# Kernel tuning notes

Measured on AMD Instinct MI355X. Metric: run time of the kernel, lower is better.

## Reference

```python
import jax, jax.numpy as jnp
import numpy as np

N_HEAD_HALF = 8          # config.n_head // 2
LAMBDA_INIT = 0.2        # diff_lambda_init
RMS_EPS = 1.1920929e-07  # torch.finfo(float32).eps (F.rms_norm default)
ROPE_BASE = 10000.0


def setup_inputs() -> dict:
    key = jax.random.key(0)
    ks = jax.random.split(key, 9)
    B, T, C = 2, 2048, 2048
    HD = C // N_HEAD_HALF  # 256
    s = 0.02
    return {
        "x": jax.random.normal(ks[0], (B, T, C), jnp.float32),
        "wq": jax.random.normal(ks[1], (C, C), jnp.float32) * s,
        "wk": jax.random.normal(ks[2], (C, C), jnp.float32) * s,
        "wv": jax.random.normal(ks[3], (C, C), jnp.float32) * s,
        "wo": jax.random.normal(ks[4], (C, C), jnp.float32) * s,
        "lq1": jax.random.normal(ks[5], (HD,), jnp.float32) * 0.1,
        "lk1": jax.random.normal(ks[6], (HD,), jnp.float32) * 0.1,
        "lq2": jax.random.normal(ks[7], (HD,), jnp.float32) * 0.1,
        "lk2": jax.random.normal(ks[8], (HD,), jnp.float32) * 0.1,
    }


def _rms_norm(x):
    var = jnp.mean(x * x, axis=-1, keepdims=True)
    return x * jax.lax.rsqrt(var + RMS_EPS)


def _rotary(x):
    # Faithful to original bug: positions run along axis 1 (the HEAD axis),
    # since Rotary is applied after transpose(1,2). x: (B, NH, T, D)
    d = x.shape[-1]
    inv_freq = (1.0 / ROPE_BASE) ** (jnp.arange(0, d, 2, dtype=jnp.float32) / d)
    t = jnp.arange(x.shape[1], dtype=jnp.float32)
    freqs = jnp.outer(t, inv_freq)                      # (NH, d/2)
    cos = jnp.cos(freqs)[None, :, None, :]
    sin = jnp.sin(freqs)[None, :, None, :]
    x1, x2 = jnp.split(x, 2, axis=-1)
    return jnp.concatenate((x1 * cos + x2 * sin, -x1 * sin + x2 * cos), axis=-1)


def _causal_attn(q, k, v, scale):
    # q,k: (B,NH,T,Dh)  v: (B,NH,T,HD)
    T = q.shape[2]
    s = jnp.einsum("bhqd,bhkd->bhqk", q, k) * scale
    mask = jnp.tril(jnp.ones((T, T), dtype=bool))
    s = jnp.where(mask, s, jnp.float32(-jnp.inf))
    p = jax.nn.softmax(s, axis=-1)
    return jnp.einsum("bhqk,bhkd->bhqd", p, v)


def reference(x, wq, wk, wv, wo, lq1, lk1, lq2, lk2):
    B, T, C = x.shape
    NH = N_HEAD_HALF
    HD = C // NH
    HH = HD // 2

    lam1 = jnp.exp(jnp.sum(lq1 * lk1))
    lam2 = jnp.exp(jnp.sum(lq2 * lk2))
    lam = lam1 - lam2 + LAMBDA_INIT

    q = (x @ wq.T).reshape(B, T, NH, 2, HH).transpose(0, 2, 1, 3, 4)
    k = (x @ wk.T).reshape(B, T, NH, 2, HH).transpose(0, 2, 1, 3, 4)
    v = (x @ wv.T).reshape(B, T, NH, HD).transpose(0, 2, 1, 3)

    q1 = _rotary(_rms_norm(q[..., 0, :]))
    q2 = _rotary(_rms_norm(q[..., 1, :]))
    k1 = _rotary(_rms_norm(k[..., 0, :]))
    k2 = _rotary(_rms_norm(k[..., 1, :]))

    scale = 1.0 / jnp.sqrt(jnp.float32(HH))
    y = _causal_attn(q1, k1, v, scale) - lam * _causal_attn(q2, k2, v, scale)

    y = y.transpose(0, 2, 1, 3).reshape(B, T, C)
    y = (y @ wo.T) * (1.0 - LAMBDA_INIT)
    return y
```

## Files before the change

kernel.cpp:

```cpp
#include <hip/hip_runtime.h>
#include <hip/hip_bf16.h>

using bf16 = __hip_bfloat16;
typedef __bf16 bf16x8_t __attribute__((ext_vector_type(8)));
typedef __bf16 bf16x4_t __attribute__((ext_vector_type(4)));
typedef float f32x4  __attribute__((ext_vector_type(4)));
typedef float f32x16 __attribute__((ext_vector_type(16)));

#define AS1 __attribute__((address_space(1)))
#define AS3 __attribute__((address_space(3)))

__device__ __forceinline__ void gll16(const void* g, void* l) {
  __builtin_amdgcn_global_load_lds((const AS1 void*)g, (AS3 void*)l, 16u, 0, 0u);
}

__device__ __forceinline__ __bf16 tobf(float f) {
  bf16 h = __float2bfloat16(f);
  return __builtin_bit_cast(__bf16, h);
}

__global__ __launch_bounds__(256) void k_cvt(
    const float* __restrict__ x,  const float* __restrict__ wq,
    const float* __restrict__ wk, const float* __restrict__ wv,
    const float* __restrict__ wo,
    bf16* __restrict__ xb,  bf16* __restrict__ wqb, bf16* __restrict__ wkb,
    bf16* __restrict__ wvb, bf16* __restrict__ wob) {
  size_t id = (size_t)blockIdx.x * 256 + threadIdx.x;
  const float* s; bf16* d; size_t off;
  if (id < 2097152) { s = x; d = xb; off = id; }
  else {
    size_t r = id - 2097152;
    unsigned w = (unsigned)(r >> 20);
    off = r & 1048575u;
    s = (w == 0) ? wq : (w == 1) ? wk : (w == 2) ? wv : wo;
    d = (w == 0) ? wqb : (w == 1) ? wkb : (w == 2) ? wvb : wob;
  }
  const float4 v = ((const float4*)s)[off];
  bf16x4_t o = { tobf(v.x), tobf(v.y), tobf(v.z), tobf(v.w) };
  *(bf16x4_t*)(d + off * 4) = o;
}

__global__ __launch_bounds__(256) void k_lam(
    const float* __restrict__ lq1, const float* __restrict__ lk1,
    const float* __restrict__ lq2, const float* __restrict__ lk2,
    float* __restrict__ lam) {
  __shared__ float r1[4], r2[4];
  int t = threadIdx.x;
  float a = lq1[t] * lk1[t];
  float b = lq2[t] * lk2[t];
#pragma unroll
  for (int s = 1; s < 64; s <<= 1) { a += __shfl_xor(a, s); b += __shfl_xor(b, s); }
  if ((t & 63) == 0) { r1[t >> 6] = a; r2[t >> 6] = b; }
  __syncthreads();
  if (t == 0) {
    float s1 = r1[0] + r1[1] + r1[2] + r1[3];
    float s2 = r2[0] + r2[1] + r2[2] + r2[3];
    *lam = expf(s1) - expf(s2) + 0.2f;
  }
}

#define MFMA16(a, b, c) __builtin_amdgcn_mfma_f32_16x16x32_bf16(a, b, c, 0, 0, 0)

template<bool SWAP>
__device__ __forceinline__ void gemm256(
    const bf16* __restrict__ A, const bf16* __restrict__ B,
    int m0, int n0, bf16* lds, f32x4 (&acc)[8][4]) {
  const int tid = threadIdx.x, lane = tid & 63;
  const int wave = tid >> 6, m = wave >> 2, n = wave & 3;
  const int g = lane >> 4, l15 = lane & 15, l7 = lane & 7;

  const int sid0 = tid, sid1 = tid + 512;
  const int sr0 = sid0 >> 3, sc0 = (sid0 & 7) ^ (sr0 & 7);
  const int sr1 = sid1 >> 3, sc1 = (sid1 & 7) ^ (sr1 & 7);

  auto stageA = [&](int t, int h) {
    bf16* d = lds + ((size_t)((t & 1) * 2 + h)) * 8192;
    gll16(A + (size_t)(m0 + h * 128 + sr0) * 2048 + t * 64 + sc0 * 8, d + sid0 * 8);
    gll16(A + (size_t)(m0 + h * 128 + sr1) * 2048 + t * 64 + sc1 * 8, d + sid1 * 8);
  };
  auto stageB = [&](int t, int h) {
    bf16* d = lds + 32768 + ((size_t)((t & 1) * 2 + h)) * 8192;
    gll16(B + (size_t)(n0 + h * 128 + sr0) * 2048 + t * 64 + sc0 * 8, d + sid0 * 8);
    gll16(B + (size_t)(n0 + h * 128 + sr1) * 2048 + t * 64 + sc1 * 8, d + sid1 * 8);
  };

  stageA(0, 0); stageB(0, 0); stageB(0, 1); stageA(0, 1);
  stageA(1, 0); stageB(1, 0); stageB(1, 1);
  asm volatile("s_waitcnt vmcnt(6)\n\ts_barrier" ::: "memory");

  for (int t = 0; t < 32; ++t) {
    const bf16* lA0 = lds + ((size_t)((t & 1) * 2 + 0)) * 8192;
    const bf16* lA1 = lds + ((size_t)((t & 1) * 2 + 1)) * 8192;
    const bf16* lB0 = lds + 32768 + ((size_t)((t & 1) * 2 + 0)) * 8192;
    const bf16* lB1 = lds + 32768 + ((size_t)((t & 1) * 2 + 1)) * 8192;
    bf16x8_t afl[4][2], afh[4][2], bvl[2][2], bvh[2][2];

#pragma unroll
    for (int ks = 0; ks < 2; ++ks) {
      const int pc = ((ks * 4 + g) ^ l7) * 8;
#pragma unroll
      for (int rf = 0; rf < 4; ++rf)
        afl[rf][ks] = *(const bf16x8_t*)(lA0 + (m * 64 + rf * 16 + l15) * 64 + pc);
#pragma unroll
      for (int cf = 0; cf < 2; ++cf)
        bvl[cf][ks] = *(const bf16x8_t*)(lB0 + (cf * 64 + n * 16 + l15) * 64 + pc);
    }
    if (t + 1 < 32) stageA(t + 1, 1);
    asm volatile("s_barrier" ::: "memory");
    __builtin_amdgcn_s_setprio(1);
#pragma unroll
    for (int ks = 0; ks < 2; ++ks)
#pragma unroll
      for (int rf = 0; rf < 4; ++rf)
#pragma unroll
        for (int cf = 0; cf < 2; ++cf)
          acc[rf][cf] = SWAP ? MFMA16(bvl[cf][ks], afl[rf][ks], acc[rf][cf])
                             : MFMA16(afl[rf][ks], bvl[cf][ks], acc[rf][cf]);
    __builtin_amdgcn_s_setprio(0);
    asm volatile("s_barrier" ::: "memory");

#pragma unroll
    for (int ks = 0; ks < 2; ++ks) {
      const int pc = ((ks * 4 + g) ^ l7) * 8;
#pragma unroll
      for (int cf = 0; cf < 2; ++cf)
        bvh[cf][ks] = *(const bf16x8_t*)(lB1 + (cf * 64 + n * 16 + l15) * 64 + pc);
    }
    if (t + 2 < 32) stageA(t + 2, 0);
    asm volatile("s_barrier" ::: "memory");
    __builtin_amdgcn_s_setprio(1);
#pragma unroll
    for (int ks = 0; ks < 2; ++ks)
#pragma unroll
      for (int rf = 0; rf < 4; ++rf)
#pragma unroll
        for (int cf = 0; cf < 2; ++cf)
          acc[rf][cf + 2] = SWAP ? MFMA16(bvh[cf][ks], afl[rf][ks], acc[rf][cf + 2])
                                 : MFMA16(afl[rf][ks], bvh[cf][ks], acc[rf][cf + 2]);
    __builtin_amdgcn_s_setprio(0);
    asm volatile("s_barrier" ::: "memory");

#pragma unroll
    for (int ks = 0; ks < 2; ++ks) {
      const int pc = ((ks * 4 + g) ^ l7) * 8;
#pragma unroll
      for (int rf = 0; rf < 4; ++rf)
        afh[rf][ks] = *(const bf16x8_t*)(lA1 + (m * 64 + rf * 16 + l15) * 64 + pc);
    }
    if (t + 2 < 32) stageB(t + 2, 0);
    asm volatile("s_barrier" ::: "memory");
    __builtin_amdgcn_s_setprio(1);
#pragma unroll
    for (int ks = 0; ks < 2; ++ks)
#pragma unroll
      for (int rf = 0; rf < 4; ++rf)
#pragma unroll
        for (int cf = 0; cf < 2; ++cf)
          acc[rf + 4][cf + 2] = SWAP ? MFMA16(bvh[cf][ks], afh[rf][ks], acc[rf + 4][cf + 2])
                                     : MFMA16(afh[rf][ks], bvh[cf][ks], acc[rf + 4][cf + 2]);
    __builtin_amdgcn_s_setprio(0);
    asm volatile("s_barrier" ::: "memory");

    if (t + 2 < 32) stageB(t + 2, 1);
    asm volatile("s_barrier" ::: "memory");
    __builtin_amdgcn_s_setprio(1);
#pragma unroll
    for (int ks = 0; ks < 2; ++ks)
#pragma unroll
      for (int rf = 0; rf < 4; ++rf)
#pragma unroll
        for (int cf = 0; cf < 2; ++cf)
          acc[rf + 4][cf] = SWAP ? MFMA16(bvl[cf][ks], afh[rf][ks], acc[rf + 4][cf])
                                 : MFMA16(afh[rf][ks], bvl[cf][ks], acc[rf + 4][cf]);
    __builtin_amdgcn_s_setprio(0);
    if (t < 30)      asm volatile("s_waitcnt vmcnt(6)\n\ts_barrier" ::: "memory");
    else             asm volatile("s_waitcnt vmcnt(0)\n\ts_barrier" ::: "memory");
  }
}

__global__ __launch_bounds__(512, 2) void k_gemm_qkv(
    const bf16* __restrict__ xb,
    const bf16* __restrict__ wqb, const bf16* __restrict__ wkb,
    const bf16* __restrict__ wvb,
    bf16* __restrict__ q1, bf16* __restrict__ q2,
    bf16* __restrict__ k1, bf16* __restrict__ k2,
    bf16* __restrict__ vt) {
  __shared__ __align__(16) bf16 lds[65536];
  __shared__ float exs[2][4][256];
  __shared__ float lCs[64], lSn[64];
  const int z  = blockIdx.z;
  const int m0 = blockIdx.y * 256, n0 = blockIdx.x * 256;
  const int nh = blockIdx.x;
  const int tid = threadIdx.x, lane = tid & 63, wave = tid >> 6;
  const int m = wave >> 2, n = wave & 3;
  const int g = lane >> 4, l15 = lane & 15;
  f32x4 acc[8][4] = {};

  if (z < 2) {
    if (tid < 64) {
      float fr = exp2f(-(float)tid * 0.20762050593045951f);
      float sn, cs;
      sincosf((float)nh * fr, &sn, &cs);
      lCs[tid] = cs; lSn[tid] = sn;
    }
    const bf16* Bm = z ? wkb : wqb;
    gemm256<true>(xb, Bm, m0, n0, lds, acc);

#pragma unroll
    for (int rf = 0; rf < 8; ++rf) {
      float s0 = 0.f, s1 = 0.f;
#pragma unroll
      for (int r = 0; r < 4; ++r) {
        s0 += acc[rf][0][r] * acc[rf][0][r] + acc[rf][1][r] * acc[rf][1][r];
        s1 += acc[rf][2][r] * acc[rf][2][r] + acc[rf][3][r] * acc[rf][3][r];
      }
      s0 += __shfl_xor(s0, 16); s0 += __shfl_xor(s0, 32);
      s1 += __shfl_xor(s1, 16); s1 += __shfl_xor(s1, 32);
      const int rrow = (rf >> 2) * 128 + m * 64 + (rf & 3) * 16 + l15;
      if (g == 0) { exs[0][n][rrow] = s0; exs[1][n][rrow] = s1; }
    }
    __syncthreads();
    bf16* dst1 = z ? k1 : q1;
    bf16* dst2 = z ? k2 : q2;
    const int j = n * 16 + 4 * g;
#pragma unroll
    for (int rf = 0; rf < 8; ++rf) {
      const int rrow = (rf >> 2) * 128 + m * 64 + (rf & 3) * 16 + l15;
      const float t0 = exs[0][0][rrow] + exs[0][1][rrow] + exs[0][2][rrow] + exs[0][3][rrow];
      const float t1 = exs[1][0][rrow] + exs[1][1][rrow] + exs[1][2][rrow] + exs[1][3][rrow];
      const float inv0 = rsqrtf(t0 * (1.0f / 128.0f) + 1.1920929e-07f);
      const float inv1 = rsqrtf(t1 * (1.0f / 128.0f) + 1.1920929e-07f);
      const size_t base = ((size_t)(m0 + rrow) * 8 + nh) * 128;
      bf16x4_t o1a, o2a, o1b, o2b;
#pragma unroll
      for (int r = 0; r < 4; ++r) {
        const float cs = lCs[j + r], sn = lSn[j + r];
        float x1 = acc[rf][0][r] * inv0, x2 = acc[rf][1][r] * inv0;
        o1a[r] = tobf(x1 * cs + x2 * sn);
        o2a[r] = tobf(x2 * cs - x1 * sn);
        x1 = acc[rf][2][r] * inv1; x2 = acc[rf][3][r] * inv1;
        o1b[r] = tobf(x1 * cs + x2 * sn);
        o2b[r] = tobf(x2 * cs - x1 * sn);
      }
      *(bf16x4_t*)(dst1 + base + j)      = o1a;
      *(bf16x4_t*)(dst1 + base + j + 64) = o2a;
      *(bf16x4_t*)(dst2 + base + j)      = o1b;
      *(bf16x4_t*)(dst2 + base + j + 64) = o2b;
    }
  } else {
    gemm256<false>(xb, wvb, m0, n0, lds, acc);
#pragma unroll
    for (int rf = 0; rf < 8; ++rf)
#pragma unroll
      for (int cf = 0; cf < 4; ++cf) {
        const int rb = m0 + (rf >> 2) * 128 + m * 64 + (rf & 3) * 16 + 4 * g;
        const int hd = (cf & 1) * 64 + (cf >> 1) * 128 + n * 16 + l15;
        const int b = rb >> 11, t = rb & 2047;
        bf16x4_t pv;
#pragma unroll
        for (int r = 0; r < 4; ++r) pv[r] = tobf(acc[rf][cf][r]);
        *(bf16x4_t*)(vt + ((size_t)((b * 8 + nh) * 256 + hd)) * 2048 + t) = pv;
      }
  }
}

template<bool SWAP>
__device__ __forceinline__ void gemm_core(
    const bf16* __restrict__ A, const bf16* __restrict__ Bm,
    int m0, int n0, bf16* lA, bf16* lB, f32x4 (&acc)[4][4]) {
  const int tid  = threadIdx.x;
  const int lane = tid & 63;
  const int g    = lane >> 4;
  const int l15  = lane & 15;
  const int l7   = lane & 7;
  const int wave = tid >> 6;
  const int wm   = (wave >> 1) * 64;
  const int wn   = (wave & 1) * 64;

  int srow[4], ssc[4];
#pragma unroll
  for (int j = 0; j < 4; ++j) {
    int id = tid + j * 256;
    srow[j] = id >> 3;
    ssc[j]  = (id & 7) ^ (srow[j] & 7);
  }

  for (int k0 = 0; k0 < 2048; k0 += 64) {
    __syncthreads();
#pragma unroll
    for (int j = 0; j < 4; ++j) {
      int id = tid + j * 256;
      gll16(A  + (size_t)(m0 + srow[j]) * 2048 + k0 + ssc[j] * 8, lA + id * 8);
      gll16(Bm + (size_t)(n0 + srow[j]) * 2048 + k0 + ssc[j] * 8, lB + id * 8);
    }
    __syncthreads();
#pragma unroll
    for (int ks = 0; ks < 2; ++ks) {
      const int pc = (ks * 4 + g) ^ l7;
      bf16x8_t af[4], bfr[4];
#pragma unroll
      for (int mt = 0; mt < 4; ++mt)
        af[mt] = *(const bf16x8_t*)(lA + (wm + mt * 16 + l15) * 64 + pc * 8);
#pragma unroll
      for (int nt = 0; nt < 4; ++nt)
        bfr[nt] = *(const bf16x8_t*)(lB + (wn + nt * 16 + l15) * 64 + pc * 8);
#pragma unroll
      for (int mt = 0; mt < 4; ++mt)
#pragma unroll
        for (int nt = 0; nt < 4; ++nt) {
          if (SWAP)
            acc[mt][nt] = MFMA16(bfr[nt], af[mt], acc[mt][nt]);
          else
            acc[mt][nt] = MFMA16(af[mt], bfr[nt], acc[mt][nt]);
        }
    }
  }
}

__global__ __launch_bounds__(256) void k_gemm_out(
    const bf16* __restrict__ yb, const bf16* __restrict__ wob,
    float* __restrict__ outp) {
  __shared__ __align__(16) bf16 lA[128 * 64];
  __shared__ __align__(16) bf16 lB[128 * 64];
  const int m0 = blockIdx.y * 128, n0 = blockIdx.x * 128;
  f32x4 acc[4][4] = {};
  gemm_core<true>(yb, wob, m0, n0, lA, lB, acc);
  const int lane = threadIdx.x & 63, wave = threadIdx.x >> 6;
  const int g = lane >> 4, l15 = lane & 15;
  const int wm = (wave >> 1) * 64, wn = (wave & 1) * 64;
#pragma unroll
  for (int mt = 0; mt < 4; ++mt)
#pragma unroll
    for (int nt = 0; nt < 4; ++nt) {
      int row = m0 + wm + mt * 16 + l15;
      int col = n0 + wn + nt * 16 + 4 * g;
      f32x4 v;
#pragma unroll
      for (int r = 0; r < 4; ++r) v[r] = acc[mt][nt][r] * 0.8f;
      *(f32x4*)(outp + (size_t)row * 2048 + col) = v;
    }
}

__global__ __launch_bounds__(256, 1) void k_flash(
    const bf16* __restrict__ q1b, const bf16* __restrict__ q2b,
    const bf16* __restrict__ k1b, const bf16* __restrict__ k2b,
    const bf16* __restrict__ vtb, const float* __restrict__ lamp,
    bf16* __restrict__ yb) {
  __shared__ __align__(16) bf16 smem[65536];
  const int tid  = threadIdx.x;
  const int lane = tid & 63, wave = tid >> 6;
  const int pair = blockIdx.x;
  const int bh = blockIdx.y;
  const int b = bh >> 3, nh = bh & 7;
  const int at = wave & 1, qg = wave >> 1;
  const int l31 = lane & 31, g5 = lane >> 5, l7 = lane & 7;
  const float scale = 0.08838834764831845f;
  const float lam = *lamp;

  auto stage = [&](int kt, int buf) {
    bf16* dst = smem + buf * 32768;
    const int k0 = kt * 64;
#pragma unroll
    for (int it = 0; it < 4; ++it) {
      int id = tid + it * 256;
      int row = id >> 4, c = id & 15;
      int sc = (c & 8) | ((c & 7) ^ (row & 7));
      size_t goff = ((size_t)(b * 2048 + k0 + row) * 8 + nh) * 128 + sc * 8;
      gll16(k1b + goff, dst + id * 8);
      gll16(k2b + goff, dst + 8192 + id * 8);
    }
#pragma unroll
    for (int it = 0; it < 8; ++it) {
      int id = tid + it * 256;
      int row = id >> 3, c = id & 7;
      int sc = c ^ (row & 7);
      gll16(vtb + ((size_t)(bh * 256 + row)) * 2048 + k0 + sc * 8,
            dst + 16384 + id * 8);
    }
  };

  bf16x8_t qf[8];
  auto loadQ = [&](int qt) {
    int qglob = qt * 64 + qg * 32 + l31;
    const bf16* qp = (at ? q2b : q1b) +
                     ((size_t)(b * 2048 + qglob) * 8 + nh) * 128 + g5 * 8;
#pragma unroll
    for (int ks = 0; ks < 8; ++ks) qf[ks] = *(const bf16x8_t*)(qp + ks * 16);
  };

  f32x16 O[8];
  float mrun, lrun;
  auto resetO = [&]() {
#pragma unroll
    for (int i = 0; i < 8; ++i)
#pragma unroll
      for (int j = 0; j < 16; ++j) O[i][j] = 0.f;
    mrun = -1e30f; lrun = 0.f;
  };

  auto step = [&](int kt, int buf, int qt) {
    const bf16* lk = smem + buf * 32768 + (at ? 8192 : 0);
    const bf16* lv = smem + buf * 32768 + 16384;
    const int k0 = kt * 64;
    const int qglob = qt * 64 + qg * 32 + l31;

    f32x16 s0, s1;
#pragma unroll
    for (int j = 0; j < 16; ++j) { s0[j] = 0.f; s1[j] = 0.f; }
#pragma unroll
    for (int ks = 0; ks < 8; ++ks) {
      int cl = ks * 2 + g5;
      int pc = (cl & 8) | ((cl & 7) ^ l7);
      bf16x8_t a0 = *(const bf16x8_t*)(lk + l31 * 128 + pc * 8);
      bf16x8_t a1 = *(const bf16x8_t*)(lk + (32 + l31) * 128 + pc * 8);
      s0 = __builtin_amdgcn_mfma_f32_32x32x16_bf16(a0, qf[ks], s0, 0, 0, 0);
      s1 = __builtin_amdgcn_mfma_f32_32x32x16_bf16(a1, qf[ks], s1, 0, 0, 0);
    }

    const bool diag = (kt == qt);
    float rmax = -3.0e38f;
#pragma unroll
    for (int r = 0; r < 16; ++r) {
      int key0 = k0 + (r & 3) + 8 * (r >> 2) + 4 * g5;
      float v0 = s0[r] * scale;
      float v1 = s1[r] * scale;
      if (diag) {
        if (key0 > qglob)      v0 = -1e30f;
        if (key0 + 32 > qglob) v1 = -1e30f;
      }
      s0[r] = v0; s1[r] = v1;
      rmax = fmaxf(rmax, fmaxf(v0, v1));
    }
    rmax = fmaxf(rmax, __shfl_xor(rmax, 32));
    float mnew = fmaxf(mrun, rmax);
    float alpha = __expf(mrun - mnew);
    float psum = 0.f;
#pragma unroll
    for (int r = 0; r < 16; ++r) {
      float p0 = __expf(s0[r] - mnew);
      float p1 = __expf(s1[r] - mnew);
      s0[r] = p0; s1[r] = p1;
      psum += p0 + p1;
    }
    psum += __shfl_xor(psum, 32);
    lrun = lrun * alpha + psum;
    mrun = mnew;
#pragma unroll
    for (int i = 0; i < 8; ++i) O[i] *= alpha;

#pragma unroll
    for (int sl = 0; sl < 4; ++sl) {
      const int h = sl & 1;
      bf16x4_t lo, hi;
#pragma unroll
      for (int j = 0; j < 4; ++j) {
        float vl = (sl < 2) ? s0[h * 8 + j]     : s1[h * 8 + j];
        float vh = (sl < 2) ? s0[h * 8 + 4 + j] : s1[h * 8 + 4 + j];
        lo[j] = tobf(vl); hi[j] = tobf(vh);
      }
      bf16x4_t send = g5 ? lo : hi;
      int2 si = __builtin_bit_cast(int2, send);
      int2 ri;
      ri.x = __shfl_xor(si.x, 32);
      ri.y = __shfl_xor(si.y, 32);
      bf16x4_t recv = __builtin_bit_cast(bf16x4_t, ri);
      bf16x4_t f0 = g5 ? recv : lo;
      bf16x4_t f1 = g5 ? hi : recv;
      bf16x8_t pf = { f0[0], f0[1], f0[2], f0[3], f1[0], f1[1], f1[2], f1[3] };

      const int cl = sl * 2 + g5;
#pragma unroll
      for (int mt = 0; mt < 8; ++mt) {
        bf16x8_t vf = *(const bf16x8_t*)(lv + (mt * 32 + l31) * 64 + (cl ^ l7) * 8);
        O[mt] = __builtin_amdgcn_mfma_f32_32x32x16_bf16(vf, pf, O[mt], 0, 0, 0);
      }
    }
  };

  auto finish = [&](int qt, bf16* cb) {
    const int qglob = qt * 64 + qg * 32 + l31;
    const float invl = 1.f / lrun;
    __syncthreads();
    if (at) {
      const float f = lam * invl;
#pragma unroll
      for (int mt = 0; mt < 8; ++mt)
#pragma unroll
        for (int rq = 0; rq < 4; ++rq) {
          int hd = mt * 32 + 8 * rq + 4 * g5;
          bf16x4_t pv;
#pragma unroll
          for (int i = 0; i < 4; ++i) pv[i] = tobf(O[mt][rq * 4 + i] * f);
          *(bf16x4_t*)(cb + (size_t)(qg * 32 + l31) * 264 + hd) = pv;
        }
    }
    __syncthreads();
    if (!at) {
#pragma unroll
      for (int mt = 0; mt < 8; ++mt)
#pragma unroll
        for (int rq = 0; rq < 4; ++rq) {
          int hd = mt * 32 + 8 * rq + 4 * g5;
          bf16x4_t o2 = *(const bf16x4_t*)(cb + (size_t)(qg * 32 + l31) * 264 + hd);
          bf16x4_t pv;
#pragma unroll
          for (int i = 0; i < 4; ++i)
            pv[i] = tobf(O[mt][rq * 4 + i] * invl - (float)o2[i]);
          *(bf16x4_t*)(yb + (size_t)(b * 2048 + qglob) * 2048 + nh * 256 + hd) = pv;
        }
    }
  };

  const int qtB = 31 - pair, qtA = pair;

  loadQ(qtB);
  resetO();
  stage(0, 0);
  for (int kt = 0; kt <= qtB; ++kt) {
    __syncthreads();
    if (kt < qtB) stage(kt + 1, (kt + 1) & 1);
    else          stage(0, (kt + 1) & 1);
    step(kt, kt & 1, qtB);
  }
  finish(qtB, smem + (qtB & 1) * 32768);

  loadQ(qtA);
  resetO();
  for (int kt = 0; kt <= qtA; ++kt) {
    __syncthreads();
    if (kt < qtA) stage(kt + 1, (qtB + kt + 2) & 1);
    step(kt, (qtB + 1 + kt) & 1, qtA);
  }
  finish(qtA, smem + 32768);
}

extern "C" void kernel_launch(void* const* d_in, const int* in_sizes, int n_in,
                              void* d_out, int out_size, void* d_ws, size_t ws_size,
                              hipStream_t stream) {
  (void)in_sizes; (void)n_in; (void)out_size; (void)ws_size;
  const float* x   = (const float*)d_in[0];
  const float* wq  = (const float*)d_in[1];
  const float* wk  = (const float*)d_in[2];
  const float* wv  = (const float*)d_in[3];
  const float* wo  = (const float*)d_in[4];
  const float* lq1 = (const float*)d_in[5];
  const float* lk1 = (const float*)d_in[6];
  const float* lq2 = (const float*)d_in[7];
  const float* lk2 = (const float*)d_in[8];
  float* out = (float*)d_out;

  char* p = (char*)d_ws;
  float* lam = (float*)p;            p += 256;
  bf16* xb  = (bf16*)p;              p += (size_t)4096 * 2048 * 2;
  bf16* wqb = (bf16*)p;              p += (size_t)2048 * 2048 * 2;
  bf16* wkb = (bf16*)p;              p += (size_t)2048 * 2048 * 2;
  bf16* wvb = (bf16*)p;              p += (size_t)2048 * 2048 * 2;
  bf16* wob = (bf16*)p;              p += (size_t)2048 * 2048 * 2;
  bf16* vt  = (bf16*)p;              p += (size_t)4096 * 2048 * 2;
  bf16* q1b = (bf16*)p;              p += (size_t)4096 * 1024 * 2;
  bf16* q2b = (bf16*)p;              p += (size_t)4096 * 1024 * 2;
  bf16* k1b = (bf16*)p;              p += (size_t)4096 * 1024 * 2;
  bf16* k2b = (bf16*)p;              p += (size_t)4096 * 1024 * 2;
  bf16* yb  = (bf16*)p;              p += (size_t)4096 * 2048 * 2;

  k_cvt<<<24576, 256, 0, stream>>>(x, wq, wk, wv, wo, xb, wqb, wkb, wvb, wob);
  k_lam<<<1, 256, 0, stream>>>(lq1, lk1, lq2, lk2, lam);
  k_gemm_qkv<<<dim3(8, 16, 3), 512, 0, stream>>>(xb, wqb, wkb, wvb,
                                                 q1b, q2b, k1b, k2b, vt);
  k_flash<<<dim3(16, 16), 256, 0, stream>>>(q1b, q2b, k1b, k2b, vt, lam, yb);
  k_gemm_out<<<dim3(16, 32), 256, 0, stream>>>(yb, wob, out);
}
```

Baseline: 434.0 us.

## Split flash attention KV tile across two wave groups with lazy rescaling

Doubles the flash-attention block to 512 threads. Each 64-key tile is split into two 32-key halves handled by separate wave groups, and the two partial softmax states are merged through shared memory at the end. Adds an exp2 with the scale folded into log2e, skips fully masked half-tiles, and only rescales the running max when it grows by more than a threshold. This raises the number of waves per CU and cuts per-wave register pressure, at the cost of an extra merge with more barriers and shared-memory traffic.

```diff
diff --git a/kernel.cpp b/kernel.cpp
--- a/kernel.cpp
+++ b/kernel.cpp
@@ -341,28 +341,29 @@
     }
 }
 
-__global__ __launch_bounds__(256, 1) void k_flash(
+__global__ __launch_bounds__(512, 2) void k_flash(
     const bf16* __restrict__ q1b, const bf16* __restrict__ q2b,
     const bf16* __restrict__ k1b, const bf16* __restrict__ k2b,
     const bf16* __restrict__ vtb, const float* __restrict__ lamp,
     bf16* __restrict__ yb) {
   __shared__ __align__(16) bf16 smem[65536];
+  __shared__ float mx[8][32], lx[8][32];
   const int tid  = threadIdx.x;
   const int lane = tid & 63, wave = tid >> 6;
   const int pair = blockIdx.x;
   const int bh = blockIdx.y;
   const int b = bh >> 3, nh = bh & 7;
-  const int at = wave & 1, qg = wave >> 1;
+  const int at = wave & 1, qg = (wave >> 1) & 1, kvh = wave >> 2;
   const int l31 = lane & 31, g5 = lane >> 5, l7 = lane & 7;
-  const float scale = 0.08838834764831845f;
+  const float sl2e = 0.12751743f;
   const float lam = *lamp;
 
   auto stage = [&](int kt, int buf) {
     bf16* dst = smem + buf * 32768;
     const int k0 = kt * 64;
 #pragma unroll
-    for (int it = 0; it < 4; ++it) {
-      int id = tid + it * 256;
+    for (int it = 0; it < 2; ++it) {
+      int id = tid + it * 512;
       int row = id >> 4, c = id & 15;
       int sc = (c & 8) | ((c & 7) ^ (row & 7));
       size_t goff = ((size_t)(b * 2048 + k0 + row) * 8 + nh) * 128 + sc * 8;
@@ -370,8 +371,8 @@
       gll16(k2b + goff, dst + 8192 + id * 8);
     }
 #pragma unroll
-    for (int it = 0; it < 8; ++it) {
-      int id = tid + it * 256;
+    for (int it = 0; it < 4; ++it) {
+      int id = tid + it * 512;
       int row = id >> 3, c = id & 7;
       int sc = c ^ (row & 7);
       gll16(vtb + ((size_t)(bh * 256 + row)) * 2048 + k0 + sc * 8,
@@ -399,64 +400,61 @@
   };
 
   auto step = [&](int kt, int buf, int qt) {
+    const int k0 = kt * 64 + kvh * 32;
+    if (k0 > qt * 64 + qg * 32 + 31) return;
     const bf16* lk = smem + buf * 32768 + (at ? 8192 : 0);
     const bf16* lv = smem + buf * 32768 + 16384;
-    const int k0 = kt * 64;
     const int qglob = qt * 64 + qg * 32 + l31;
 
-    f32x16 s0, s1;
-#pragma unroll
-    for (int j = 0; j < 16; ++j) { s0[j] = 0.f; s1[j] = 0.f; }
+    f32x16 s0;
+#pragma unroll
+    for (int j = 0; j < 16; ++j) s0[j] = 0.f;
 #pragma unroll
     for (int ks = 0; ks < 8; ++ks) {
       int cl = ks * 2 + g5;
       int pc = (cl & 8) | ((cl & 7) ^ l7);
-      bf16x8_t a0 = *(const bf16x8_t*)(lk + l31 * 128 + pc * 8);
-      bf16x8_t a1 = *(const bf16x8_t*)(lk + (32 + l31) * 128 + pc * 8);
+      bf16x8_t a0 = *(const bf16x8_t*)(lk + (kvh * 32 + l31) * 128 + pc * 8);
       s0 = __builtin_amdgcn_mfma_f32_32x32x16_bf16(a0, qf[ks], s0, 0, 0, 0);
-      s1 = __builtin_amdgcn_mfma_f32_32x32x16_bf16(a1, qf[ks], s1, 0, 0, 0);
-    }
-
-    const bool diag = (kt == qt);
+    }
+
+    const bool needmask = (k0 + 31 > qt * 64 + qg * 32);
     float rmax = -3.0e38f;
 #pragma unroll
     for (int r = 0; r < 16; ++r) {
-      int key0 = k0 + (r & 3) + 8 * (r >> 2) + 4 * g5;
-      float v0 = s0[r] * scale;
-      float v1 = s1[r] * scale;
-      if (diag) {
-        if (key0 > qglob)      v0 = -1e30f;
-        if (key0 + 32 > qglob) v1 = -1e30f;
-      }
-      s0[r] = v0; s1[r] = v1;
-      rmax = fmaxf(rmax, fmaxf(v0, v1));
+      float v0 = s0[r] * sl2e;
+      if (needmask) {
+        int key0 = k0 + (r & 3) + 8 * (r >> 2) + 4 * g5;
+        if (key0 > qglob) v0 = -1e30f;
+      }
+      s0[r] = v0;
+      rmax = fmaxf(rmax, v0);
     }
     rmax = fmaxf(rmax, __shfl_xor(rmax, 32));
-    float mnew = fmaxf(mrun, rmax);
-    float alpha = __expf(mrun - mnew);
+    if (!__all(rmax - mrun <= 8.0f)) {
+      float mnew = fmaxf(mrun, rmax);
+      float alpha = exp2f(mrun - mnew);
+      lrun *= alpha;
+#pragma unroll
+      for (int i = 0; i < 8; ++i) O[i] *= alpha;
+      mrun = mnew;
+    }
     float psum = 0.f;
 #pragma unroll
     for (int r = 0; r < 16; ++r) {
-      float p0 = __expf(s0[r] - mnew);
-      float p1 = __expf(s1[r] - mnew);
-      s0[r] = p0; s1[r] = p1;
-      psum += p0 + p1;
+      float p0 = exp2f(s0[r] - mrun);
+      s0[r] = p0;
+      psum += p0;
     }
     psum += __shfl_xor(psum, 32);
-    lrun = lrun * alpha + psum;
-    mrun = mnew;
-#pragma unroll
-    for (int i = 0; i < 8; ++i) O[i] *= alpha;
-
-#pragma unroll
-    for (int sl = 0; sl < 4; ++sl) {
-      const int h = sl & 1;
+    lrun += psum;
+
+#pragma unroll
+    for (int sl = 0; sl < 2; ++sl) {
       bf16x4_t lo, hi;
 #pragma unroll
       for (int j = 0; j < 4; ++j) {
-        float vl = (sl < 2) ? s0[h * 8 + j]     : s1[h * 8 + j];
-        float vh = (sl < 2) ? s0[h * 8 + 4 + j] : s1[h * 8 + 4 + j];
-        lo[j] = tobf(vl); hi[j] = tobf(vh);
+        lo[j] = tobf(s0[sl * 8 + j]);
+        hi[j] = tobf(s0[sl * 8 + 4 + j]);
       }
       bf16x4_t send = g5 ? lo : hi;
       int2 si = __builtin_bit_cast(int2, send);
@@ -468,7 +466,7 @@
       bf16x4_t f1 = g5 ? hi : recv;
       bf16x8_t pf = { f0[0], f0[1], f0[2], f0[3], f1[0], f1[1], f1[2], f1[3] };
 
-      const int cl = sl * 2 + g5;
+      const int cl = kvh * 4 + sl * 2 + g5;
 #pragma unroll
       for (int mt = 0; mt < 8; ++mt) {
         bf16x8_t vf = *(const bf16x8_t*)(lv + (mt * 32 + l31) * 64 + (cl ^ l7) * 8);
@@ -477,11 +475,49 @@
     }
   };
 
-  auto finish = [&](int qt, bf16* cb) {
+  auto finish = [&](int qt, bf16* cbuf) {
     const int qglob = qt * 64 + qg * 32 + l31;
-    const float invl = 1.f / lrun;
-    __syncthreads();
-    if (at) {
+    float* XF = (float*)cbuf;
+    __syncthreads();
+    if (g5 == 0) { mx[wave][l31] = mrun; lx[wave][l31] = lrun; }
+    __syncthreads();
+    const float mo  = mx[wave ^ 4][l31];
+    const float lo2 = lx[wave ^ 4][l31];
+    const float ms = fmaxf(mrun, mo);
+    const float ws = exp2f(mrun - ms);
+    const float wo = exp2f(mo - ms);
+    const float lstar = lrun * ws + lo2 * wo;
+#pragma unroll
+    for (int rnd = 0; rnd < 2; ++rnd) {
+      if (at == rnd && kvh == 1) {
+#pragma unroll
+        for (int mt = 0; mt < 8; ++mt)
+#pragma unroll
+          for (int rq = 0; rq < 4; ++rq) {
+            int hd = mt * 32 + 8 * rq + 4 * g5;
+            f32x4 v;
+#pragma unroll
+            for (int i = 0; i < 4; ++i) v[i] = O[mt][rq * 4 + i] * ws;
+            *(f32x4*)(XF + qg * 8192 + l31 * 256 + hd) = v;
+          }
+      }
+      __syncthreads();
+      if (at == rnd && kvh == 0) {
+#pragma unroll
+        for (int mt = 0; mt < 8; ++mt)
+#pragma unroll
+          for (int rq = 0; rq < 4; ++rq) {
+            int hd = mt * 32 + 8 * rq + 4 * g5;
+            f32x4 v = *(const f32x4*)(XF + qg * 8192 + l31 * 256 + hd);
+#pragma unroll
+            for (int i = 0; i < 4; ++i)
+              O[mt][rq * 4 + i] = O[mt][rq * 4 + i] * ws + v[i];
+          }
+      }
+      __syncthreads();
+    }
+    const float invl = 1.f / lstar;
+    if (kvh == 0 && at == 1) {
       const float f = lam * invl;
 #pragma unroll
       for (int mt = 0; mt < 8; ++mt)
@@ -491,17 +527,17 @@
           bf16x4_t pv;
 #pragma unroll
           for (int i = 0; i < 4; ++i) pv[i] = tobf(O[mt][rq * 4 + i] * f);
-          *(bf16x4_t*)(cb + (size_t)(qg * 32 + l31) * 264 + hd) = pv;
+          *(bf16x4_t*)(cbuf + (size_t)(qg * 32 + l31) * 264 + hd) = pv;
         }
     }
     __syncthreads();
-    if (!at) {
+    if (kvh == 0 && at == 0) {
 #pragma unroll
       for (int mt = 0; mt < 8; ++mt)
 #pragma unroll
         for (int rq = 0; rq < 4; ++rq) {
           int hd = mt * 32 + 8 * rq + 4 * g5;
-          bf16x4_t o2 = *(const bf16x4_t*)(cb + (size_t)(qg * 32 + l31) * 264 + hd);
+          bf16x4_t o2 = *(const bf16x4_t*)(cbuf + (size_t)(qg * 32 + l31) * 264 + hd);
           bf16x4_t pv;
 #pragma unroll
           for (int i = 0; i < 4; ++i)
@@ -567,6 +603,6 @@
   k_lam<<<1, 256, 0, stream>>>(lq1, lk1, lq2, lk2, lam);
   k_gemm_qkv<<<dim3(8, 16, 3), 512, 0, stream>>>(xb, wqb, wkb, wvb,
                                                  q1b, q2b, k1b, k2b, vt);
-  k_flash<<<dim3(16, 16), 256, 0, stream>>>(q1b, q2b, k1b, k2b, vt, lam, yb);
+  k_flash<<<dim3(16, 16), 512, 0, stream>>>(q1b, q2b, k1b, k2b, vt, lam, yb);
   k_gemm_out<<<dim3(16, 32), 256, 0, stream>>>(yb, wob, out);
 }
```

Measured after the change: 425.7 us. About the same (-1.9%).
